# Optimization experiments

Measured on AMD Instinct MI355X. Metric: run time of the kernel, lower is better.

## Reference

```python
import jax, jax.numpy as jnp
import numpy as np

DIM = 512
WIN = 8
HEADS = 16
HEAD_DIM = DIM // HEADS
N = WIN * WIN
B_ = 1568


def _rel_pos_idx(window_size: int) -> np.ndarray:
    ch = np.arange(window_size)
    cw = np.arange(window_size)
    coords = np.stack(np.meshgrid(ch, cw, indexing='ij'))  # [2, W, W]
    flat = coords.reshape(2, -1)                            # [2, N]
    rel = flat[:, :, None] - flat[:, None, :]               # [2, N, N]
    rel = rel.transpose(1, 2, 0).copy()                     # [N, N, 2]
    rel[:, :, 0] += window_size - 1
    rel[:, :, 1] += window_size - 1
    rel[:, :, 0] *= 2 * window_size - 1
    return rel.sum(-1).astype(np.int32)                     # [N, N]


def setup_inputs() -> dict:
    key = jax.random.key(0)
    kx, kt, kq, kp, kb = jax.random.split(key, 5)
    x = jax.random.normal(kx, (B_, N, DIM), dtype=jnp.float32)
    # learned params
    table = jax.random.normal(kt, ((2 * WIN - 1) ** 2, HEADS), dtype=jnp.float32) * 0.02
    qkv_w = jax.random.normal(kq, (3 * DIM, DIM), dtype=jnp.float32) * (1.0 / np.sqrt(DIM))
    proj_w = jax.random.normal(kp, (DIM, DIM), dtype=jnp.float32) * (1.0 / np.sqrt(DIM))
    proj_b = jax.random.normal(kb, (DIM,), dtype=jnp.float32) * 0.02
    rel_idx = jnp.asarray(_rel_pos_idx(WIN))  # [N, N] int32
    return {"x": x, "qkv_w": qkv_w, "table": table, "proj_w": proj_w,
            "proj_b": proj_b, "rel_idx": rel_idx}


def reference(x, qkv_w, table, proj_w, proj_b, rel_idx):
    Bw, n, c = x.shape
    scale = jnp.sqrt(jnp.float32(HEAD_DIM))
    # qkv: Linear no-bias, torch weight [3C, C] -> x @ W^T
    qkv = (x @ qkv_w.T).reshape(Bw, n, 3, HEADS, HEAD_DIM)
    qkv = jnp.transpose(qkv, (2, 0, 3, 1, 4))  # [3, B, H, N, hd]
    q, k, v = qkv[0], qkv[1], qkv[2]
    attn = jnp.einsum('bhnd,bhmd->bhnm', q, k) / scale  # [B, H, N, N]
    bias = table[rel_idx]                                # [N, N, H]
    attn = attn + jnp.transpose(bias, (2, 0, 1))[None]   # [B, H, N, N]
    attn = jax.nn.softmax(attn, axis=-1)
    out = jnp.einsum('bhnm,bhmd->bhnd', attn, v)         # [B, H, N, hd]
    out = jnp.transpose(out, (0, 2, 1, 3)).reshape(Bw, n, c)
    return out @ proj_w.T + proj_b
```

## Files before the change

kernel.cpp:

```cpp
#include <hip/hip_runtime.h>
#include <stdint.h>

typedef unsigned short ushort_t;
typedef unsigned long long u64_t;
typedef __attribute__((ext_vector_type(4))) float f32x4;
typedef __attribute__((ext_vector_type(8))) short s16x8;

#define S1_ELEMS ((size_t)1568*64*512)

__device__ __forceinline__ ushort_t f2bf(float f) {
  unsigned u = __builtin_bit_cast(unsigned, f);
  u = u + 0x7fffu + ((u >> 16) & 1u);
  return (ushort_t)(u >> 16);
}

__device__ __forceinline__ void gl_lds16(const ushort_t* g, ushort_t* l) {
  typedef __attribute__((address_space(1))) void gvoid;
  typedef __attribute__((address_space(3))) void lvoid;
  __builtin_amdgcn_global_load_lds((gvoid*)(ushort_t*)g, (lvoid*)l, 16, 0, 0);
}

__global__ void k_convert_hi(const float* __restrict__ src, ushort_t* __restrict__ hi, long n4) {
  long i = (long)blockIdx.x * blockDim.x + threadIdx.x;
  long stride = (long)gridDim.x * blockDim.x;
  for (; i < n4; i += stride) {
    float4 v = ((const float4*)src)[i];
    ushort4 h;
    h.x = f2bf(v.x); h.y = f2bf(v.y); h.z = f2bf(v.z); h.w = f2bf(v.w);
    ((ushort4*)hi)[i] = h;
  }
}

__global__ void k_bias(const float* __restrict__ table, const int* __restrict__ rel_idx,
                       float* __restrict__ bias) {
  int i = blockIdx.x * 256 + threadIdx.x;
  int h = i >> 12, rc = i & 4095;
  bias[i] = table[rel_idx[rc] * 16 + h];
}

__device__ __forceinline__ void gemm256_loop(
    ushort_t* lds, const ushort_t* pA, const ushort_t* pB,
    int w, int lane, int wm, int wn, f32x4 (&acc)[8][4]) {
  #pragma unroll
  for (int q = 0; q < 2; q++) {
    gl_lds16(pA + q*8192 +  0, lds + ((2*w + q)*2 + 0)*512);
    gl_lds16(pA + q*8192 + 32, lds + ((2*w + q)*2 + 1)*512);
    gl_lds16(pB + q*8192 +  0, lds + 16384 + ((2*w + q)*2 + 0)*512);
    gl_lds16(pB + q*8192 + 32, lds + 16384 + ((2*w + q)*2 + 1)*512);
  }
  asm volatile("s_waitcnt vmcnt(0)" ::: "memory");
  __builtin_amdgcn_s_barrier();

  for (int tau = 0; tau < 8; ++tau) {
    ushort_t* bufR = lds + (tau & 1)*32768;
    ushort_t* bufW = lds + ((tau & 1) ^ 1)*32768;
    if (tau < 7) {
      int ko = (tau + 1)*64;
      #pragma unroll
      for (int q = 0; q < 2; q++) {
        gl_lds16(pA + q*8192 + ko,      bufW + ((2*w + q)*2 + 0)*512);
        gl_lds16(pA + q*8192 + ko + 32, bufW + ((2*w + q)*2 + 1)*512);
        gl_lds16(pB + q*8192 + ko,      bufW + 16384 + ((2*w + q)*2 + 0)*512);
        gl_lds16(pB + q*8192 + ko + 32, bufW + 16384 + ((2*w + q)*2 + 1)*512);
      }
    }
    s16x8 af[4][2], bf[4][2];
    #pragma unroll
    for (int t = 0; t < 4; t++)
      #pragma unroll
      for (int kh = 0; kh < 2; kh++) {
        af[t][kh] = *(const s16x8*)&bufR[((wm*8 + t)*2 + kh)*512 + lane*8];
        bf[t][kh] = *(const s16x8*)&bufR[16384 + ((wn*4 + t)*2 + kh)*512 + lane*8];
      }
    __builtin_amdgcn_s_barrier();
    asm volatile("s_waitcnt lgkmcnt(0)" ::: "memory");
    __builtin_amdgcn_sched_barrier(0);
    __builtin_amdgcn_s_setprio(1);
    #pragma unroll
    for (int t = 0; t < 4; t++)
      #pragma unroll
      for (int tb = 0; tb < 4; tb++) {
        acc[t][tb] = __builtin_amdgcn_mfma_f32_16x16x32_bf16(af[t][0], bf[tb][0], acc[t][tb], 0, 0, 0);
        acc[t][tb] = __builtin_amdgcn_mfma_f32_16x16x32_bf16(af[t][1], bf[tb][1], acc[t][tb], 0, 0, 0);
      }
    __builtin_amdgcn_s_setprio(0);
    s16x8 ag[4][2];
    #pragma unroll
    for (int t = 0; t < 4; t++)
      #pragma unroll
      for (int kh = 0; kh < 2; kh++)
        ag[t][kh] = *(const s16x8*)&bufR[((wm*8 + 4 + t)*2 + kh)*512 + lane*8];
    asm volatile("s_waitcnt lgkmcnt(0)" ::: "memory");
    __builtin_amdgcn_sched_barrier(0);
    __builtin_amdgcn_s_setprio(1);
    #pragma unroll
    for (int t = 0; t < 4; t++)
      #pragma unroll
      for (int tb = 0; tb < 4; tb++) {
        acc[4 + t][tb] = __builtin_amdgcn_mfma_f32_16x16x32_bf16(ag[t][0], bf[tb][0], acc[4 + t][tb], 0, 0, 0);
        acc[4 + t][tb] = __builtin_amdgcn_mfma_f32_16x16x32_bf16(ag[t][1], bf[tb][1], acc[4 + t][tb], 0, 0, 0);
      }
    __builtin_amdgcn_s_setprio(0);
    asm volatile("s_waitcnt vmcnt(0)" ::: "memory");
    __builtin_amdgcn_s_barrier();
  }
}

__global__ __launch_bounds__(512, 2) void k_gemm_qkv(
    const ushort_t* __restrict__ xh, const ushort_t* __restrict__ wh,
    ushort_t* __restrict__ qh, ushort_t* __restrict__ kh, ushort_t* __restrict__ vt) {
  extern __shared__ __align__(16) ushort_t lds[];
  const int tid = threadIdx.x, w = tid >> 6, lane = tid & 63;
  const int g = lane >> 4, l15 = lane & 15;
  const int wm = w >> 2, wn = w & 3;
  int flat = blockIdx.x;
  int swz = (flat & 7) * 294 + (flat >> 3);
  int bx = swz % 6, by = swz / 6;

  const ushort_t* pA = xh + ((size_t)by*256 + (size_t)(2*w)*16 + l15)*512 + g*8;
  const ushort_t* pB = wh + ((size_t)bx*256 + (size_t)(2*w)*16 + l15)*512 + g*8;

  f32x4 acc[8][4];
  #pragma unroll
  for (int r = 0; r < 8; r++)
    #pragma unroll
    for (int c = 0; c < 4; c++) acc[r][c] = (f32x4){0.f, 0.f, 0.f, 0.f};

  gemm256_loop(lds, pA, pB, w, lane, wm, wn, acc);

  asm volatile("" ::: "memory");
  const int sel = bx >> 1;
  if (sel < 2) {
    #pragma unroll
    for (int ra = 0; ra < 8; ra++)
      #pragma unroll
      for (int tb = 0; tb < 4; tb++)
        #pragma unroll
        for (int j = 0; j < 4; j++) {
          int row = wm*128 + ra*16 + g*4 + j;
          int col = wn*64 + tb*16 + l15;
          int r = (row >> 6)*8 + (col >> 5);
          int n = row & 63, d = col & 31;
          int byte = r*4096 + ((n*64 + d*2) ^ ((n & 12) << 3));
          *(ushort_t*)((char*)lds + byte) = f2bf(acc[ra][tb][j]);
        }
  } else {
    #pragma unroll
    for (int ra = 0; ra < 8; ra++)
      #pragma unroll
      for (int tb = 0; tb < 4; tb++) {
        int row0 = wm*128 + ra*16 + g*4;
        int col = wn*64 + tb*16 + l15;
        int r = (row0 >> 6)*8 + (col >> 5);
        int n0 = row0 & 63, d = col & 31;
        u64_t pk = (u64_t)f2bf(acc[ra][tb][0])
                 | ((u64_t)f2bf(acc[ra][tb][1]) << 16)
                 | ((u64_t)f2bf(acc[ra][tb][2]) << 32)
                 | ((u64_t)f2bf(acc[ra][tb][3]) << 48);
        int byte = r*4096 + ((d*128 + n0*2) ^ ((d & 7) << 4) ^ (((((d >> 3) ^ (n0 >> 3))) & 1) << 6));
        *(u64_t*)((char*)lds + byte) = pk;
      }
  }
  asm volatile("s_waitcnt lgkmcnt(0)" ::: "memory");
  __builtin_amdgcn_s_barrier();
  ushort_t* dst = (sel == 0) ? qh : (sel == 1) ? kh : vt;
  const int hbase = (bx & 1) * 8;
  #pragma unroll
  for (int it = 0; it < 16; it++) {
    int cg = it*512 + tid;
    int r = cg >> 8, inner = cg & 255;
    int byte;
    if (sel < 2) byte = r*4096 + ((inner*16) ^ (((inner >> 2) & 12) << 3));
    else         byte = r*4096 + ((inner*16) ^ (((inner >> 3) & 7) << 4) ^ ((((inner >> 6) ^ inner) & 1) << 6));
    s16x8 v = *(const s16x8*)((const char*)lds + byte);
    int b = by*4 + (r >> 3), h = hbase + (r & 7);
    *(s16x8*)&dst[(size_t)(b*16 + h)*2048 + inner*8] = v;
  }
}

__global__ __launch_bounds__(512, 2) void k_gemm_proj(
    const ushort_t* __restrict__ ah, const ushort_t* __restrict__ wh,
    const float* __restrict__ pb, float* __restrict__ out) {
  extern __shared__ __align__(16) ushort_t lds[];
  const int tid = threadIdx.x, w = tid >> 6, lane = tid & 63;
  const int g = lane >> 4, l15 = lane & 15;
  const int wm = w >> 2, wn = w & 3;
  int flat = blockIdx.x;
  int swz = (flat & 7) * 98 + (flat >> 3);
  int bx = swz & 1, by = swz >> 1;

  const ushort_t* pA = ah + ((size_t)by*256 + (size_t)(2*w)*16 + l15)*512 + g*8;
  const ushort_t* pB = wh + ((size_t)bx*256 + (size_t)(2*w)*16 + l15)*512 + g*8;

  f32x4 acc[8][4];
  #pragma unroll
  for (int r = 0; r < 8; r++)
    #pragma unroll
    for (int c = 0; c < 4; c++) acc[r][c] = (f32x4){0.f, 0.f, 0.f, 0.f};

  gemm256_loop(lds, pA, pB, w, lane, wm, wn, acc);

  asm volatile("" ::: "memory");
  #pragma unroll
  for (int p = 0; p < 2; p++) {
    if (p) { asm volatile("" ::: "memory"); __builtin_amdgcn_s_barrier(); }
    if (wm == p) {
      #pragma unroll
      for (int ra = 0; ra < 8; ra++)
        #pragma unroll
        for (int tb = 0; tb < 4; tb++)
          #pragma unroll
          for (int j = 0; j < 4; j++) {
            int row = ra*16 + g*4 + j;
            int col = wn*64 + tb*16 + l15;
            int byte = (row*1024 + col*4) ^ ((row & 12) << 2) ^ ((row & 8) << 3);
            *(float*)((char*)lds + byte) = acc[ra][tb][j];
          }
    }
    asm volatile("s_waitcnt lgkmcnt(0)" ::: "memory");
    __builtin_amdgcn_s_barrier();
    #pragma unroll
    for (int it = 0; it < 16; it++) {
      int cg = it*512 + tid;
      int row = cg >> 6, c16 = cg & 63;
      int byte = row*1024 + ((c16*16) ^ ((row & 12) << 2) ^ ((row & 8) << 3));
      f32x4 v = *(const f32x4*)((const char*)lds + byte);
      int ncol = bx*256 + c16*4;
      f32x4 pbv = *(const f32x4*)&pb[ncol];
      v = v + pbv;
      *(f32x4*)&out[(size_t)(by*256 + p*128 + row)*512 + ncol] = v;
    }
  }
}

__global__ __launch_bounds__(256) void k_attn(
    const ushort_t* __restrict__ qh, const ushort_t* __restrict__ kh,
    const ushort_t* __restrict__ vt, const float* __restrict__ bias,
    ushort_t* __restrict__ aoh) {
  __shared__ ushort_t plds[4][64*72];
  const int tid = threadIdx.x, w = tid >> 6, lane = tid & 63;
  const int g = lane >> 4, l15 = lane & 15;
  const int gw = blockIdx.x * 4 + w;
  const int b = gw >> 4, h = gw & 15;
  const size_t base = (size_t)(b*16 + h) * 2048;

  s16x8 qf[4], kf[4];
  #pragma unroll
  for (int t = 0; t < 4; t++) {
    size_t o = base + (size_t)(t*16 + l15)*32 + g*8;
    qf[t] = *(const s16x8*)&qh[o];
    kf[t] = *(const s16x8*)&kh[o];
  }
  s16x8 vf[2][2];
  #pragma unroll
  for (int kt = 0; kt < 2; kt++)
    #pragma unroll
    for (int nt = 0; nt < 2; nt++)
      vf[kt][nt] = *(const s16x8*)&vt[base + (size_t)(nt*16 + l15)*64 + kt*32 + g*8];

  f32x4 s[4][4];
  #pragma unroll
  for (int r = 0; r < 4; r++)
    #pragma unroll
    for (int c = 0; c < 4; c++) s[r][c] = (f32x4){0.f,0.f,0.f,0.f};
  #pragma unroll
  for (int r = 0; r < 4; r++)
    #pragma unroll
    for (int c = 0; c < 4; c++)
      s[r][c] = __builtin_amdgcn_mfma_f32_16x16x32_bf16(qf[r], kf[c], s[r][c], 0, 0, 0);

  const float invs = 0.17677669529663687f;
  const float* bh_ = bias + ((size_t)h << 12);
  #pragma unroll
  for (int r = 0; r < 4; r++)
    #pragma unroll
    for (int c = 0; c < 4; c++)
      #pragma unroll
      for (int j = 0; j < 4; j++) {
        int rr = r*16 + g*4 + j, cc = c*16 + l15;
        s[r][c][j] = s[r][c][j]*invs + bh_[rr*64 + cc];
      }

  #pragma unroll
  for (int r = 0; r < 4; r++)
    #pragma unroll
    for (int j = 0; j < 4; j++) {
      float mx = fmaxf(fmaxf(s[r][0][j], s[r][1][j]), fmaxf(s[r][2][j], s[r][3][j]));
      mx = fmaxf(mx, __shfl_xor(mx, 1));
      mx = fmaxf(mx, __shfl_xor(mx, 2));
      mx = fmaxf(mx, __shfl_xor(mx, 4));
      mx = fmaxf(mx, __shfl_xor(mx, 8));
      float p0 = __expf(s[r][0][j]-mx), p1 = __expf(s[r][1][j]-mx);
      float p2 = __expf(s[r][2][j]-mx), p3 = __expf(s[r][3][j]-mx);
      float sum = p0 + p1 + p2 + p3;
      sum += __shfl_xor(sum, 1);
      sum += __shfl_xor(sum, 2);
      sum += __shfl_xor(sum, 4);
      sum += __shfl_xor(sum, 8);
      float rv = 1.0f / sum;
      s[r][0][j] = p0*rv; s[r][1][j] = p1*rv; s[r][2][j] = p2*rv; s[r][3][j] = p3*rv;
    }

  ushort_t* Pm = plds[w];
  #pragma unroll
  for (int r = 0; r < 4; r++)
    #pragma unroll
    for (int c = 0; c < 4; c++)
      #pragma unroll
      for (int j = 0; j < 4; j++) {
        int rr = r*16 + g*4 + j, cc = c*16 + l15;
        Pm[rr*72 + cc] = f2bf(s[r][c][j]);
      }
  s16x8 pf[4][2];
  #pragma unroll
  for (int ta = 0; ta < 4; ta++)
    #pragma unroll
    for (int kt = 0; kt < 2; kt++)
      pf[ta][kt] = *(const s16x8*)&Pm[(ta*16 + l15)*72 + kt*32 + g*8];

  f32x4 o[4][2];
  #pragma unroll
  for (int ta = 0; ta < 4; ta++)
    #pragma unroll
    for (int nt = 0; nt < 2; nt++) o[ta][nt] = (f32x4){0.f,0.f,0.f,0.f};
  #pragma unroll
  for (int ta = 0; ta < 4; ta++)
    #pragma unroll
    for (int nt = 0; nt < 2; nt++)
      #pragma unroll
      for (int kt = 0; kt < 2; kt++)
        o[ta][nt] = __builtin_amdgcn_mfma_f32_16x16x32_bf16(pf[ta][kt], vf[kt][nt], o[ta][nt], 0, 0, 0);

  #pragma unroll
  for (int ta = 0; ta < 4; ta++)
    #pragma unroll
    for (int nt = 0; nt < 2; nt++)
      #pragma unroll
      for (int j = 0; j < 4; j++) {
        int rr = ta*16 + g*4 + j, dd = nt*16 + l15;
        aoh[((size_t)b*64 + rr)*512 + h*32 + dd] = f2bf(o[ta][nt][j]);
      }
}

extern "C" void kernel_launch(void* const* d_in, const int* in_sizes, int n_in,
                              void* d_out, int out_size, void* d_ws, size_t ws_size,
                              hipStream_t stream) {
  const float* x      = (const float*)d_in[0];
  const float* qkv_w  = (const float*)d_in[1];
  const float* table  = (const float*)d_in[2];
  const float* proj_w = (const float*)d_in[3];
  const float* proj_b = (const float*)d_in[4];
  const int*   rel_idx = (const int*)d_in[5];

  const size_t S1 = S1_ELEMS;
  const size_t need = (4*S1 + 786432 + 262144)*sizeof(ushort_t) + 65536*sizeof(float);
  if (ws_size < need) return;

  ushort_t* qh  = (ushort_t*)d_ws;
  ushort_t* kh  = qh + S1;
  ushort_t* vt  = kh + S1;
  ushort_t* xh  = vt + S1;
  ushort_t* wqh = xh + S1;
  ushort_t* wph = wqh + 786432;
  float*    bias = (float*)(wph + 262144);
  ushort_t* aoh = xh;

  hipFuncSetAttribute((const void*)k_gemm_qkv,
                      hipFuncAttributeMaxDynamicSharedMemorySize, 131072);
  hipFuncSetAttribute((const void*)k_gemm_proj,
                      hipFuncAttributeMaxDynamicSharedMemorySize, 131072);

  k_convert_hi<<<2048, 256, 0, stream>>>(x, xh, (long)(S1/4));
  k_convert_hi<<<768, 256, 0, stream>>>(qkv_w, wqh, 196608);
  k_convert_hi<<<256, 256, 0, stream>>>(proj_w, wph, 65536);
  k_bias<<<256, 256, 0, stream>>>(table, rel_idx, bias);
  k_gemm_qkv<<<2352, 512, 131072, stream>>>(xh, wqh, qh, kh, vt);
  k_attn<<<6272, 256, 0, stream>>>(qh, kh, vt, bias, aoh);
  k_gemm_proj<<<784, 512, 131072, stream>>>(aoh, wph, proj_b, (float*)d_out);
}
```

Before: 558.2 us.

## Fuse fp32-to-bf16 conversion of x into the QKV GEMM operand load

Removes the separate conversion kernel for the large input x. The QKV GEMM now loads fp32 x into registers, converts to bf16 and writes it to LDS, while the weights still stream through direct global-to-LDS loads. This avoids writing and re-reading the bf16 copy of x. In exchange, each tile re-reads fp32 x (twice the bytes) across the 6 column tiles and spends VALU work on conversion inside the pipelined loop.

```diff
diff --git a/kernel.cpp b/kernel.cpp
--- a/kernel.cpp
+++ b/kernel.cpp
@@ -107,7 +107,7 @@
 }
 
 __global__ __launch_bounds__(512, 2) void k_gemm_qkv(
-    const ushort_t* __restrict__ xh, const ushort_t* __restrict__ wh,
+    const float* __restrict__ xf, const ushort_t* __restrict__ wh,
     ushort_t* __restrict__ qh, ushort_t* __restrict__ kh, ushort_t* __restrict__ vt) {
   extern __shared__ __align__(16) ushort_t lds[];
   const int tid = threadIdx.x, w = tid >> 6, lane = tid & 63;
@@ -117,8 +117,8 @@
   int swz = (flat & 7) * 294 + (flat >> 3);
   int bx = swz % 6, by = swz / 6;
 
-  const ushort_t* pA = xh + ((size_t)by*256 + (size_t)(2*w)*16 + l15)*512 + g*8;
-  const ushort_t* pB = wh + ((size_t)bx*256 + (size_t)(2*w)*16 + l15)*512 + g*8;
+  const float*    pAf = xf + (size_t)(by*256 + 32*w + l15)*512 + g*8;
+  const ushort_t* pB  = wh + ((size_t)bx*256 + (size_t)(32*w) + l15)*512 + g*8;
 
   f32x4 acc[8][4];
   #pragma unroll
@@ -126,7 +126,109 @@
     #pragma unroll
     for (int c = 0; c < 4; c++) acc[r][c] = (f32x4){0.f, 0.f, 0.f, 0.f};
 
-  gemm256_loop(lds, pA, pB, w, lane, wm, wn, acc);
+  f32x4 a0[4], a1[4];
+
+  #pragma unroll
+  for (int q = 0; q < 2; q++)
+    #pragma unroll
+    for (int kh2 = 0; kh2 < 2; kh2++) {
+      const float* p = pAf + q*8192 + kh2*32;
+      a0[q*2 + kh2] = *(const f32x4*)p;
+      a1[q*2 + kh2] = *(const f32x4*)(p + 4);
+    }
+  gl_lds16(pB +        0, lds + 16384 + ((2*w + 0)*2 + 0)*512);
+  gl_lds16(pB +       32, lds + 16384 + ((2*w + 0)*2 + 1)*512);
+  gl_lds16(pB + 8192 + 0, lds + 16384 + ((2*w + 1)*2 + 0)*512);
+  gl_lds16(pB + 8192 +32, lds + 16384 + ((2*w + 1)*2 + 1)*512);
+  #pragma unroll
+  for (int q = 0; q < 2; q++)
+    #pragma unroll
+    for (int kh2 = 0; kh2 < 2; kh2++) {
+      int i = q*2 + kh2;
+      s16x8 pk;
+      #pragma unroll
+      for (int j = 0; j < 4; j++) {
+        pk[j]     = (short)f2bf(a0[i][j]);
+        pk[4 + j] = (short)f2bf(a1[i][j]);
+      }
+      *(s16x8*)&lds[((2*w + q)*2 + kh2)*512 + lane*8] = pk;
+    }
+  asm volatile("s_waitcnt vmcnt(0) lgkmcnt(0)" ::: "memory");
+  __builtin_amdgcn_s_barrier();
+
+  for (int tau = 0; tau < 8; ++tau) {
+    ushort_t* bufR = lds + (tau & 1)*32768;
+    ushort_t* bufW = lds + ((tau & 1) ^ 1)*32768;
+    if (tau < 7) {
+      int ko = (tau + 1)*64;
+      #pragma unroll
+      for (int q = 0; q < 2; q++)
+        #pragma unroll
+        for (int kh2 = 0; kh2 < 2; kh2++) {
+          const float* p = pAf + q*8192 + ko + kh2*32;
+          a0[q*2 + kh2] = *(const f32x4*)p;
+          a1[q*2 + kh2] = *(const f32x4*)(p + 4);
+        }
+      gl_lds16(pB + ko,            bufW + 16384 + ((2*w + 0)*2 + 0)*512);
+      gl_lds16(pB + ko + 32,       bufW + 16384 + ((2*w + 0)*2 + 1)*512);
+      gl_lds16(pB + 8192 + ko,     bufW + 16384 + ((2*w + 1)*2 + 0)*512);
+      gl_lds16(pB + 8192 + ko +32, bufW + 16384 + ((2*w + 1)*2 + 1)*512);
+    }
+    s16x8 af[4][2], bf[4][2];
+    #pragma unroll
+    for (int t = 0; t < 4; t++)
+      #pragma unroll
+      for (int kh2 = 0; kh2 < 2; kh2++) {
+        af[t][kh2] = *(const s16x8*)&bufR[((wm*8 + t)*2 + kh2)*512 + lane*8];
+        bf[t][kh2] = *(const s16x8*)&bufR[16384 + ((wn*4 + t)*2 + kh2)*512 + lane*8];
+      }
+    __builtin_amdgcn_s_barrier();
+    asm volatile("s_waitcnt lgkmcnt(0)" ::: "memory");
+    __builtin_amdgcn_sched_barrier(0);
+    __builtin_amdgcn_s_setprio(1);
+    #pragma unroll
+    for (int t = 0; t < 4; t++)
+      #pragma unroll
+      for (int tb = 0; tb < 4; tb++) {
+        acc[t][tb] = __builtin_amdgcn_mfma_f32_16x16x32_bf16(af[t][0], bf[tb][0], acc[t][tb], 0, 0, 0);
+        acc[t][tb] = __builtin_amdgcn_mfma_f32_16x16x32_bf16(af[t][1], bf[tb][1], acc[t][tb], 0, 0, 0);
+      }
+    __builtin_amdgcn_s_setprio(0);
+    s16x8 ag[4][2];
+    #pragma unroll
+    for (int t = 0; t < 4; t++)
+      #pragma unroll
+      for (int kh2 = 0; kh2 < 2; kh2++)
+        ag[t][kh2] = *(const s16x8*)&bufR[((wm*8 + 4 + t)*2 + kh2)*512 + lane*8];
+    asm volatile("s_waitcnt lgkmcnt(0)" ::: "memory");
+    __builtin_amdgcn_sched_barrier(0);
+    __builtin_amdgcn_s_setprio(1);
+    #pragma unroll
+    for (int t = 0; t < 4; t++)
+      #pragma unroll
+      for (int tb = 0; tb < 4; tb++) {
+        acc[4 + t][tb] = __builtin_amdgcn_mfma_f32_16x16x32_bf16(ag[t][0], bf[tb][0], acc[4 + t][tb], 0, 0, 0);
+        acc[4 + t][tb] = __builtin_amdgcn_mfma_f32_16x16x32_bf16(ag[t][1], bf[tb][1], acc[4 + t][tb], 0, 0, 0);
+      }
+    __builtin_amdgcn_s_setprio(0);
+    if (tau < 7) {
+      #pragma unroll
+      for (int q = 0; q < 2; q++)
+        #pragma unroll
+        for (int kh2 = 0; kh2 < 2; kh2++) {
+          int i = q*2 + kh2;
+          s16x8 pk;
+          #pragma unroll
+          for (int j = 0; j < 4; j++) {
+            pk[j]     = (short)f2bf(a0[i][j]);
+            pk[4 + j] = (short)f2bf(a1[i][j]);
+          }
+          *(s16x8*)&bufW[((2*w + q)*2 + kh2)*512 + lane*8] = pk;
+        }
+    }
+    asm volatile("s_waitcnt vmcnt(0) lgkmcnt(0)" ::: "memory");
+    __builtin_amdgcn_s_barrier();
+  }
 
   asm volatile("" ::: "memory");
   const int sel = bx >> 1;
@@ -359,22 +461,20 @@
   ushort_t* qh  = (ushort_t*)d_ws;
   ushort_t* kh  = qh + S1;
   ushort_t* vt  = kh + S1;
-  ushort_t* xh  = vt + S1;
-  ushort_t* wqh = xh + S1;
+  ushort_t* aoh = vt + S1;
+  ushort_t* wqh = aoh + S1;
   ushort_t* wph = wqh + 786432;
   float*    bias = (float*)(wph + 262144);
-  ushort_t* aoh = xh;
 
   hipFuncSetAttribute((const void*)k_gemm_qkv,
                       hipFuncAttributeMaxDynamicSharedMemorySize, 131072);
   hipFuncSetAttribute((const void*)k_gemm_proj,
                       hipFuncAttributeMaxDynamicSharedMemorySize, 131072);
 
-  k_convert_hi<<<2048, 256, 0, stream>>>(x, xh, (long)(S1/4));
   k_convert_hi<<<768, 256, 0, stream>>>(qkv_w, wqh, 196608);
   k_convert_hi<<<256, 256, 0, stream>>>(proj_w, wph, 65536);
   k_bias<<<256, 256, 0, stream>>>(table, rel_idx, bias);
-  k_gemm_qkv<<<2352, 512, 131072, stream>>>(xh, wqh, qh, kh, vt);
+  k_gemm_qkv<<<2352, 512, 131072, stream>>>(x, wqh, qh, kh, vt);
   k_attn<<<6272, 256, 0, stream>>>(qh, kh, vt, bias, aoh);
   k_gemm_proj<<<784, 512, 131072, stream>>>(aoh, wph, proj_b, (float*)d_out);
 }
```

Measured after the change: 582.2 us. 1.04x slower.

## Halve QKV GEMM LDS footprint with K=32 stages and two-pass epilogue

Applied to the files above, without the earlier changes.

The QKV GEMM now stages K in chunks of 32 instead of 64, halving dynamic LDS from 128KB to 64KB, and requests launch bounds of 4 blocks per CU. To fit the epilogue into the smaller LDS, the output transpose is split into two passes, one per wm half, with an extra barrier between them. The fp32-to-bf16 convert kernel also processes 8 elements per thread with a 16-byte store. The aim is higher occupancy and latency hiding in the GEMM. In exchange it adds twice as many K-loop iterations and barriers, and register pressure under the tighter launch bound may cause spills.

```diff
diff --git a/kernel.cpp b/kernel.cpp
--- a/kernel.cpp
+++ b/kernel.cpp
@@ -20,14 +20,18 @@
   __builtin_amdgcn_global_load_lds((gvoid*)(ushort_t*)g, (lvoid*)l, 16, 0, 0);
 }
 
-__global__ void k_convert_hi(const float* __restrict__ src, ushort_t* __restrict__ hi, long n4) {
+__global__ void k_convert_hi(const float* __restrict__ src, ushort_t* __restrict__ hi, long n8) {
   long i = (long)blockIdx.x * blockDim.x + threadIdx.x;
   long stride = (long)gridDim.x * blockDim.x;
-  for (; i < n4; i += stride) {
-    float4 v = ((const float4*)src)[i];
-    ushort4 h;
-    h.x = f2bf(v.x); h.y = f2bf(v.y); h.z = f2bf(v.z); h.w = f2bf(v.w);
-    ((ushort4*)hi)[i] = h;
+  for (; i < n8; i += stride) {
+    float4 v0 = ((const float4*)src)[2*i];
+    float4 v1 = ((const float4*)src)[2*i + 1];
+    s16x8 pk;
+    pk[0] = (short)f2bf(v0.x); pk[1] = (short)f2bf(v0.y);
+    pk[2] = (short)f2bf(v0.z); pk[3] = (short)f2bf(v0.w);
+    pk[4] = (short)f2bf(v1.x); pk[5] = (short)f2bf(v1.y);
+    pk[6] = (short)f2bf(v1.z); pk[7] = (short)f2bf(v1.w);
+    *(s16x8*)&hi[i*8] = pk;
   }
 }
 
@@ -38,75 +42,7 @@
   bias[i] = table[rel_idx[rc] * 16 + h];
 }
 
-__device__ __forceinline__ void gemm256_loop(
-    ushort_t* lds, const ushort_t* pA, const ushort_t* pB,
-    int w, int lane, int wm, int wn, f32x4 (&acc)[8][4]) {
-  #pragma unroll
-  for (int q = 0; q < 2; q++) {
-    gl_lds16(pA + q*8192 +  0, lds + ((2*w + q)*2 + 0)*512);
-    gl_lds16(pA + q*8192 + 32, lds + ((2*w + q)*2 + 1)*512);
-    gl_lds16(pB + q*8192 +  0, lds + 16384 + ((2*w + q)*2 + 0)*512);
-    gl_lds16(pB + q*8192 + 32, lds + 16384 + ((2*w + q)*2 + 1)*512);
-  }
-  asm volatile("s_waitcnt vmcnt(0)" ::: "memory");
-  __builtin_amdgcn_s_barrier();
-
-  for (int tau = 0; tau < 8; ++tau) {
-    ushort_t* bufR = lds + (tau & 1)*32768;
-    ushort_t* bufW = lds + ((tau & 1) ^ 1)*32768;
-    if (tau < 7) {
-      int ko = (tau + 1)*64;
-      #pragma unroll
-      for (int q = 0; q < 2; q++) {
-        gl_lds16(pA + q*8192 + ko,      bufW + ((2*w + q)*2 + 0)*512);
-        gl_lds16(pA + q*8192 + ko + 32, bufW + ((2*w + q)*2 + 1)*512);
-        gl_lds16(pB + q*8192 + ko,      bufW + 16384 + ((2*w + q)*2 + 0)*512);
-        gl_lds16(pB + q*8192 + ko + 32, bufW + 16384 + ((2*w + q)*2 + 1)*512);
-      }
-    }
-    s16x8 af[4][2], bf[4][2];
-    #pragma unroll
-    for (int t = 0; t < 4; t++)
-      #pragma unroll
-      for (int kh = 0; kh < 2; kh++) {
-        af[t][kh] = *(const s16x8*)&bufR[((wm*8 + t)*2 + kh)*512 + lane*8];
-        bf[t][kh] = *(const s16x8*)&bufR[16384 + ((wn*4 + t)*2 + kh)*512 + lane*8];
-      }
-    __builtin_amdgcn_s_barrier();
-    asm volatile("s_waitcnt lgkmcnt(0)" ::: "memory");
-    __builtin_amdgcn_sched_barrier(0);
-    __builtin_amdgcn_s_setprio(1);
-    #pragma unroll
-    for (int t = 0; t < 4; t++)
-      #pragma unroll
-      for (int tb = 0; tb < 4; tb++) {
-        acc[t][tb] = __builtin_amdgcn_mfma_f32_16x16x32_bf16(af[t][0], bf[tb][0], acc[t][tb], 0, 0, 0);
-        acc[t][tb] = __builtin_amdgcn_mfma_f32_16x16x32_bf16(af[t][1], bf[tb][1], acc[t][tb], 0, 0, 0);
-      }
-    __builtin_amdgcn_s_setprio(0);
-    s16x8 ag[4][2];
-    #pragma unroll
-    for (int t = 0; t < 4; t++)
-      #pragma unroll
-      for (int kh = 0; kh < 2; kh++)
-        ag[t][kh] = *(const s16x8*)&bufR[((wm*8 + 4 + t)*2 + kh)*512 + lane*8];
-    asm volatile("s_waitcnt lgkmcnt(0)" ::: "memory");
-    __builtin_amdgcn_sched_barrier(0);
-    __builtin_amdgcn_s_setprio(1);
-    #pragma unroll
-    for (int t = 0; t < 4; t++)
-      #pragma unroll
-      for (int tb = 0; tb < 4; tb++) {
-        acc[4 + t][tb] = __builtin_amdgcn_mfma_f32_16x16x32_bf16(ag[t][0], bf[tb][0], acc[4 + t][tb], 0, 0, 0);
-        acc[4 + t][tb] = __builtin_amdgcn_mfma_f32_16x16x32_bf16(ag[t][1], bf[tb][1], acc[4 + t][tb], 0, 0, 0);
-      }
-    __builtin_amdgcn_s_setprio(0);
-    asm volatile("s_waitcnt vmcnt(0)" ::: "memory");
-    __builtin_amdgcn_s_barrier();
-  }
-}
-
-__global__ __launch_bounds__(512, 2) void k_gemm_qkv(
+__global__ __launch_bounds__(512, 4) void k_gemm_qkv(
     const ushort_t* __restrict__ xh, const ushort_t* __restrict__ wh,
     ushort_t* __restrict__ qh, ushort_t* __restrict__ kh, ushort_t* __restrict__ vt) {
   extern __shared__ __align__(16) ushort_t lds[];
@@ -117,8 +53,8 @@
   int swz = (flat & 7) * 294 + (flat >> 3);
   int bx = swz % 6, by = swz / 6;
 
-  const ushort_t* pA = xh + ((size_t)by*256 + (size_t)(2*w)*16 + l15)*512 + g*8;
-  const ushort_t* pB = wh + ((size_t)bx*256 + (size_t)(2*w)*16 + l15)*512 + g*8;
+  const ushort_t* pA = xh + ((size_t)by*256 + (size_t)(32*w) + l15)*512 + g*8;
+  const ushort_t* pB = wh + ((size_t)bx*256 + (size_t)(32*w) + l15)*512 + g*8;
 
   f32x4 acc[8][4];
   #pragma unroll
@@ -126,55 +62,176 @@
     #pragma unroll
     for (int c = 0; c < 4; c++) acc[r][c] = (f32x4){0.f, 0.f, 0.f, 0.f};
 
-  gemm256_loop(lds, pA, pB, w, lane, wm, wn, acc);
-
-  asm volatile("" ::: "memory");
+  gl_lds16(pA,        lds + (2*w)*512);
+  gl_lds16(pA + 8192, lds + (2*w + 1)*512);
+  gl_lds16(pB,        lds + 8192 + (2*w)*512);
+  gl_lds16(pB + 8192, lds + 8192 + (2*w + 1)*512);
+  asm volatile("s_waitcnt vmcnt(0)" ::: "memory");
+  __builtin_amdgcn_s_barrier();
+
+  for (int tau = 0; tau < 16; ++tau) {
+    ushort_t* bufR = lds + (tau & 1)*16384;
+    ushort_t* bufW = lds + ((tau & 1) ^ 1)*16384;
+    if (tau < 15) {
+      int ko = (tau + 1)*32;
+      gl_lds16(pA + ko,        bufW + (2*w)*512);
+      gl_lds16(pA + 8192 + ko, bufW + (2*w + 1)*512);
+      gl_lds16(pB + ko,        bufW + 8192 + (2*w)*512);
+      gl_lds16(pB + 8192 + ko, bufW + 8192 + (2*w + 1)*512);
+    }
+    s16x8 af[4], bf[4];
+    #pragma unroll
+    for (int t = 0; t < 4; t++) {
+      af[t] = *(const s16x8*)&bufR[(wm*8 + t)*512 + lane*8];
+      bf[t] = *(const s16x8*)&bufR[8192 + (wn*4 + t)*512 + lane*8];
+    }
+    __builtin_amdgcn_s_barrier();
+    asm volatile("s_waitcnt lgkmcnt(0)" ::: "memory");
+    __builtin_amdgcn_sched_barrier(0);
+    __builtin_amdgcn_s_setprio(1);
+    #pragma unroll
+    for (int t = 0; t < 4; t++)
+      #pragma unroll
+      for (int tb = 0; tb < 4; tb++)
+        acc[t][tb] = __builtin_amdgcn_mfma_f32_16x16x32_bf16(af[t], bf[tb], acc[t][tb], 0, 0, 0);
+    __builtin_amdgcn_s_setprio(0);
+    s16x8 ag[4];
+    #pragma unroll
+    for (int t = 0; t < 4; t++)
+      ag[t] = *(const s16x8*)&bufR[(wm*8 + 4 + t)*512 + lane*8];
+    asm volatile("s_waitcnt lgkmcnt(0)" ::: "memory");
+    __builtin_amdgcn_sched_barrier(0);
+    __builtin_amdgcn_s_setprio(1);
+    #pragma unroll
+    for (int t = 0; t < 4; t++)
+      #pragma unroll
+      for (int tb = 0; tb < 4; tb++)
+        acc[4 + t][tb] = __builtin_amdgcn_mfma_f32_16x16x32_bf16(ag[t], bf[tb], acc[4 + t][tb], 0, 0, 0);
+    __builtin_amdgcn_s_setprio(0);
+    asm volatile("s_waitcnt vmcnt(0)" ::: "memory");
+    __builtin_amdgcn_s_barrier();
+  }
+
   const int sel = bx >> 1;
-  if (sel < 2) {
-    #pragma unroll
-    for (int ra = 0; ra < 8; ra++)
-      #pragma unroll
-      for (int tb = 0; tb < 4; tb++)
-        #pragma unroll
-        for (int j = 0; j < 4; j++) {
-          int row = wm*128 + ra*16 + g*4 + j;
-          int col = wn*64 + tb*16 + l15;
-          int r = (row >> 6)*8 + (col >> 5);
-          int n = row & 63, d = col & 31;
-          int byte = r*4096 + ((n*64 + d*2) ^ ((n & 12) << 3));
-          *(ushort_t*)((char*)lds + byte) = f2bf(acc[ra][tb][j]);
-        }
-  } else {
-    #pragma unroll
-    for (int ra = 0; ra < 8; ra++)
-      #pragma unroll
-      for (int tb = 0; tb < 4; tb++) {
-        int row0 = wm*128 + ra*16 + g*4;
-        int col = wn*64 + tb*16 + l15;
-        int r = (row0 >> 6)*8 + (col >> 5);
-        int n0 = row0 & 63, d = col & 31;
-        u64_t pk = (u64_t)f2bf(acc[ra][tb][0])
-                 | ((u64_t)f2bf(acc[ra][tb][1]) << 16)
-                 | ((u64_t)f2bf(acc[ra][tb][2]) << 32)
-                 | ((u64_t)f2bf(acc[ra][tb][3]) << 48);
-        int byte = r*4096 + ((d*128 + n0*2) ^ ((d & 7) << 4) ^ (((((d >> 3) ^ (n0 >> 3))) & 1) << 6));
-        *(u64_t*)((char*)lds + byte) = pk;
-      }
-  }
-  asm volatile("s_waitcnt lgkmcnt(0)" ::: "memory");
-  __builtin_amdgcn_s_barrier();
   ushort_t* dst = (sel == 0) ? qh : (sel == 1) ? kh : vt;
   const int hbase = (bx & 1) * 8;
   #pragma unroll
-  for (int it = 0; it < 16; it++) {
-    int cg = it*512 + tid;
-    int r = cg >> 8, inner = cg & 255;
-    int byte;
-    if (sel < 2) byte = r*4096 + ((inner*16) ^ (((inner >> 2) & 12) << 3));
-    else         byte = r*4096 + ((inner*16) ^ (((inner >> 3) & 7) << 4) ^ ((((inner >> 6) ^ inner) & 1) << 6));
-    s16x8 v = *(const s16x8*)((const char*)lds + byte);
-    int b = by*4 + (r >> 3), h = hbase + (r & 7);
-    *(s16x8*)&dst[(size_t)(b*16 + h)*2048 + inner*8] = v;
+  for (int p = 0; p < 2; p++) {
+    if (p) { asm volatile("" ::: "memory"); __builtin_amdgcn_s_barrier(); }
+    if (wm == p) {
+      if (sel < 2) {
+        #pragma unroll
+        for (int ra = 0; ra < 8; ra++)
+          #pragma unroll
+          for (int tb = 0; tb < 4; tb++)
+            #pragma unroll
+            for (int j = 0; j < 4; j++) {
+              int lr = ra*16 + g*4 + j;
+              int col = wn*64 + tb*16 + l15;
+              int r = (lr >> 6)*8 + (col >> 5);
+              int n = lr & 63, d = col & 31;
+              int byte = r*4096 + ((n*64 + d*2) ^ ((n & 12) << 3));
+              *(ushort_t*)((char*)lds + byte) = f2bf(acc[ra][tb][j]);
+            }
+      } else {
+        #pragma unroll
+        for (int ra = 0; ra < 8; ra++)
+          #pragma unroll
+          for (int tb = 0; tb < 4; tb++) {
+            int lr0 = ra*16 + g*4;
+            int col = wn*64 + tb*16 + l15;
+            int r = (lr0 >> 6)*8 + (col >> 5);
+            int n0 = lr0 & 63, d = col & 31;
+            u64_t pk = (u64_t)f2bf(acc[ra][tb][0])
+                     | ((u64_t)f2bf(acc[ra][tb][1]) << 16)
+                     | ((u64_t)f2bf(acc[ra][tb][2]) << 32)
+                     | ((u64_t)f2bf(acc[ra][tb][3]) << 48);
+            int byte = r*4096 + ((d*128 + n0*2) ^ ((d & 7) << 4) ^ (((((d >> 3) ^ (n0 >> 3))) & 1) << 6));
+            *(u64_t*)((char*)lds + byte) = pk;
+          }
+      }
+    }
+    asm volatile("s_waitcnt lgkmcnt(0)" ::: "memory");
+    __builtin_amdgcn_s_barrier();
+    #pragma unroll
+    for (int it = 0; it < 8; it++) {
+      int cg = it*512 + tid;
+      int r = cg >> 8, inner = cg & 255;
+      int byte;
+      if (sel < 2) byte = r*4096 + ((inner*16) ^ (((inner >> 2) & 12) << 3));
+      else         byte = r*4096 + ((inner*16) ^ (((inner >> 3) & 7) << 4) ^ ((((inner >> 6) ^ inner) & 1) << 6));
+      s16x8 v = *(const s16x8*)((const char*)lds + byte);
+      int b = by*4 + p*2 + (r >> 3), h = hbase + (r & 7);
+      *(s16x8*)&dst[(size_t)(b*16 + h)*2048 + inner*8] = v;
+    }
+  }
+}
+
+__device__ __forceinline__ void gemm256_loop(
+    ushort_t* lds, const ushort_t* pA, const ushort_t* pB,
+    int w, int lane, int wm, int wn, f32x4 (&acc)[8][4]) {
+  #pragma unroll
+  for (int q = 0; q < 2; q++) {
+    gl_lds16(pA + q*8192 +  0, lds + ((2*w + q)*2 + 0)*512);
+    gl_lds16(pA + q*8192 + 32, lds + ((2*w + q)*2 + 1)*512);
+    gl_lds16(pB + q*8192 +  0, lds + 16384 + ((2*w + q)*2 + 0)*512);
+    gl_lds16(pB + q*8192 + 32, lds + 16384 + ((2*w + q)*2 + 1)*512);
+  }
+  asm volatile("s_waitcnt vmcnt(0)" ::: "memory");
+  __builtin_amdgcn_s_barrier();
+
+  for (int tau = 0; tau < 8; ++tau) {
+    ushort_t* bufR = lds + (tau & 1)*32768;
+    ushort_t* bufW = lds + ((tau & 1) ^ 1)*32768;
+    if (tau < 7) {
+      int ko = (tau + 1)*64;
+      #pragma unroll
+      for (int q = 0; q < 2; q++) {
+        gl_lds16(pA + q*8192 + ko,      bufW + ((2*w + q)*2 + 0)*512);
+        gl_lds16(pA + q*8192 + ko + 32, bufW + ((2*w + q)*2 + 1)*512);
+        gl_lds16(pB + q*8192 + ko,      bufW + 16384 + ((2*w + q)*2 + 0)*512);
+        gl_lds16(pB + q*8192 + ko + 32, bufW + 16384 + ((2*w + q)*2 + 1)*512);
+      }
+    }
+    s16x8 af[4][2], bf[4][2];
+    #pragma unroll
+    for (int t = 0; t < 4; t++)
+      #pragma unroll
+      for (int kh = 0; kh < 2; kh++) {
+        af[t][kh] = *(const s16x8*)&bufR[((wm*8 + t)*2 + kh)*512 + lane*8];
+        bf[t][kh] = *(const s16x8*)&bufR[16384 + ((wn*4 + t)*2 + kh)*512 + lane*8];
+      }
+    __builtin_amdgcn_s_barrier();
+    asm volatile("s_waitcnt lgkmcnt(0)" ::: "memory");
+    __builtin_amdgcn_sched_barrier(0);
+    __builtin_amdgcn_s_setprio(1);
+    #pragma unroll
+    for (int t = 0; t < 4; t++)
+      #pragma unroll
+      for (int tb = 0; tb < 4; tb++) {
+        acc[t][tb] = __builtin_amdgcn_mfma_f32_16x16x32_bf16(af[t][0], bf[tb][0], acc[t][tb], 0, 0, 0);
+        acc[t][tb] = __builtin_amdgcn_mfma_f32_16x16x32_bf16(af[t][1], bf[tb][1], acc[t][tb], 0, 0, 0);
+      }
+    __builtin_amdgcn_s_setprio(0);
+    s16x8 ag[4][2];
+    #pragma unroll
+    for (int t = 0; t < 4; t++)
+      #pragma unroll
+      for (int kh = 0; kh < 2; kh++)
+        ag[t][kh] = *(const s16x8*)&bufR[((wm*8 + 4 + t)*2 + kh)*512 + lane*8];
+    asm volatile("s_waitcnt lgkmcnt(0)" ::: "memory");
+    __builtin_amdgcn_sched_barrier(0);
+    __builtin_amdgcn_s_setprio(1);
+    #pragma unroll
+    for (int t = 0; t < 4; t++)
+      #pragma unroll
+      for (int tb = 0; tb < 4; tb++) {
+        acc[4 + t][tb] = __builtin_amdgcn_mfma_f32_16x16x32_bf16(ag[t][0], bf[tb][0], acc[4 + t][tb], 0, 0, 0);
+        acc[4 + t][tb] = __builtin_amdgcn_mfma_f32_16x16x32_bf16(ag[t][1], bf[tb][1], acc[4 + t][tb], 0, 0, 0);
+      }
+    __builtin_amdgcn_s_setprio(0);
+    asm volatile("s_waitcnt vmcnt(0)" ::: "memory");
+    __builtin_amdgcn_s_barrier();
   }
 }
 
@@ -366,15 +423,15 @@
   ushort_t* aoh = xh;
 
   hipFuncSetAttribute((const void*)k_gemm_qkv,
-                      hipFuncAttributeMaxDynamicSharedMemorySize, 131072);
+                      hipFuncAttributeMaxDynamicSharedMemorySize, 65536);
   hipFuncSetAttribute((const void*)k_gemm_proj,
                       hipFuncAttributeMaxDynamicSharedMemorySize, 131072);
 
-  k_convert_hi<<<2048, 256, 0, stream>>>(x, xh, (long)(S1/4));
-  k_convert_hi<<<768, 256, 0, stream>>>(qkv_w, wqh, 196608);
-  k_convert_hi<<<256, 256, 0, stream>>>(proj_w, wph, 65536);
+  k_convert_hi<<<3136, 256, 0, stream>>>(x, xh, (long)(S1/8));
+  k_convert_hi<<<384, 256, 0, stream>>>(qkv_w, wqh, 98304);
+  k_convert_hi<<<128, 256, 0, stream>>>(proj_w, wph, 32768);
   k_bias<<<256, 256, 0, stream>>>(table, rel_idx, bias);
-  k_gemm_qkv<<<2352, 512, 131072, stream>>>(xh, wqh, qh, kh, vt);
+  k_gemm_qkv<<<2352, 512, 65536, stream>>>(xh, wqh, qh, kh, vt);
   k_attn<<<6272, 256, 0, stream>>>(qh, kh, vt, bias, aoh);
   k_gemm_proj<<<784, 512, 131072, stream>>>(aoh, wph, proj_b, (float*)d_out);
 }
```

Result: slower. 1.604 ms (+187.4%).
